# Kernel tuning notes

Hardware: AMD Instinct MI355X
Metric: run time of the kernel (lower is better)

Reference implementation:

```python
import jax, jax.numpy as jnp
import numpy as np

B, L, D, H = 4, 1024, 1024, 16
HS = D // H
BLOCK = 1024
EPS = 1e-5


def setup_inputs() -> dict:
    key = jax.random.key(0)
    ks = jax.random.split(key, 12)
    s = 0.02
    return {
        "x": jax.random.normal(ks[0], (B, L, D), jnp.float32),
        "ln1_w": jnp.ones((D,), jnp.float32),
        "ln1_b": jnp.zeros((D,), jnp.float32),
        "Wqkv": jax.random.normal(ks[1], (D, 3 * D), jnp.float32) * s,
        "bqkv": jnp.zeros((3 * D,), jnp.float32),
        "Wproj": jax.random.normal(ks[2], (D, D), jnp.float32) * s,
        "bproj": jnp.zeros((D,), jnp.float32),
        "Er": jax.random.normal(ks[3], (BLOCK, HS), jnp.float32) * s,
        "ln2_w": jnp.ones((D,), jnp.float32),
        "ln2_b": jnp.zeros((D,), jnp.float32),
        "Wfc": jax.random.normal(ks[4], (D, 4 * D), jnp.float32) * s,
        "bfc": jnp.zeros((4 * D,), jnp.float32),
        "Wfc2": jax.random.normal(ks[5], (4 * D, D), jnp.float32) * s,
        "bfc2": jnp.zeros((D,), jnp.float32),
    }


def _layernorm(x, w, b):
    mu = jnp.mean(x, axis=-1, keepdims=True)
    var = jnp.mean(jnp.square(x - mu), axis=-1, keepdims=True)
    return (x - mu) * jax.lax.rsqrt(var + EPS) * w + b


def _skew(QEr):
    # Music-Transformer skew: pad one zero column on the left of last dim,
    # reshape (B,H,L,L+1) -> (B,H,L+1,L), drop first row.
    b, h, l, _ = QEr.shape
    padded = jnp.pad(QEr, ((0, 0), (0, 0), (0, 0), (1, 0)))
    return padded.reshape(b, h, l + 1, l)[:, :, 1:, :]


def _block(x, ln1_w, ln1_b, Wqkv, bqkv, Wproj, bproj, Er,
           ln2_w, ln2_b, Wfc, bfc, Wfc2, bfc2):
    b, l, d = x.shape
    # --- attention on ln_1(x) ---
    h = _layernorm(x, ln1_w, ln1_b)
    qkv = h @ Wqkv + bqkv                      # (B, L, 3D)
    q, k, v = jnp.split(qkv, 3, axis=-1)
    q = q.reshape(b, l, H, HS).transpose(0, 2, 1, 3)  # (B,H,L,hs)
    k = k.reshape(b, l, H, HS).transpose(0, 2, 1, 3)
    v = v.reshape(b, l, H, HS).transpose(0, 2, 1, 3)

    start = BLOCK - l
    Er_t = Er[start:, :].T                     # (hs, L)
    QEr = jnp.einsum('bhld,dm->bhlm', q, Er_t)  # (B,H,L,L)
    Srel = _skew(QEr)

    QKt = jnp.einsum('bhld,bhmd->bhlm', q, k)  # (B,H,L,L)
    scale = 1.0 / jnp.sqrt(jnp.asarray(HS, x.dtype))
    att = (QKt + Srel) * scale
    causal = jnp.tril(jnp.ones((l, l), bool))
    att = jnp.where(causal, att, jnp.asarray(-jnp.inf, att.dtype))
    att = jax.nn.softmax(att, axis=-1)
    y = jnp.einsum('bhlm,bhmd->bhld', att, v)  # (B,H,L,hs)
    y = y.transpose(0, 2, 1, 3).reshape(b, l, d)
    a = y @ Wproj + bproj

    x = x + a
    # --- MLP on ln_2(x) ---
    h2 = _layernorm(x, ln2_w, ln2_b)
    m = jax.nn.gelu(h2 @ Wfc + bfc, approximate=False) @ Wfc2 + bfc2
    return x + m


def reference(x, ln1_w, ln1_b, Wqkv, bqkv, Wproj, bproj, Er,
              ln2_w, ln2_b, Wfc, bfc, Wfc2, bfc2):
    return _block(x, ln1_w, ln1_b, Wqkv, bqkv, Wproj, bproj, Er,
                  ln2_w, ln2_b, Wfc, bfc, Wfc2, bfc2)
```

## Files before the change

### kernel.cpp

```cpp
#include <hip/hip_runtime.h>
#include <hip/hip_bf16.h>
#include <math.h>

typedef __attribute__((ext_vector_type(8))) __bf16 bf16x8;
typedef __attribute__((ext_vector_type(4))) float f32x4;

#define LL 1024
#define DD 1024
#define HH 16

#define GLOAD16(g, l)                                              \
  __builtin_amdgcn_global_load_lds(                                \
      (const __attribute__((address_space(1))) void*)(g),          \
      (__attribute__((address_space(3))) void*)(l), 16, 0, 0)

#define FENCE asm volatile("" ::: "memory")
#define BARRIER do { FENCE; __builtin_amdgcn_s_barrier(); FENCE; } while (0)
#define SCHEDB __builtin_amdgcn_sched_barrier(0)

__global__ __launch_bounds__(256) void transpose_cvt(const float* __restrict__ W,
                                                     __hip_bfloat16* __restrict__ Wt,
                                                     int R, int C) {
  __shared__ float tile[32][33];
  int tx = threadIdx.x;
  int r0 = blockIdx.y * 32, c0 = blockIdx.x * 32;
  int r = tx >> 3, c4 = (tx & 7) * 4;
  float4 v = *(const float4*)&W[(size_t)(r0 + r) * C + c0 + c4];
  tile[r][c4 + 0] = v.x; tile[r][c4 + 1] = v.y;
  tile[r][c4 + 2] = v.z; tile[r][c4 + 3] = v.w;
  __syncthreads();
  int c = tx >> 3, r4 = (tx & 7) * 4;
  __hip_bfloat16 o[4];
#pragma unroll
  for (int j = 0; j < 4; ++j) o[j] = __float2bfloat16(tile[r4 + j][c]);
  *(uint2*)&Wt[(size_t)(c0 + c) * R + r0 + r4] = *(const uint2*)o;
}

__global__ __launch_bounds__(256) void cvt_er(const float* __restrict__ Er,
                                              __hip_bfloat16* __restrict__ Erb) {
  int i = blockIdx.x * 256 + threadIdx.x;
  float4 v = *(const float4*)&Er[(size_t)i * 4];
  __hip_bfloat16 o[4];
  o[0] = __float2bfloat16(v.x); o[1] = __float2bfloat16(v.y);
  o[2] = __float2bfloat16(v.z); o[3] = __float2bfloat16(v.w);
  *(uint2*)&Erb[(size_t)i * 4] = *(const uint2*)o;
}

__global__ __launch_bounds__(256) void ln_kernel(const float* __restrict__ X,
                                                 const float* __restrict__ w,
                                                 const float* __restrict__ b,
                                                 __hip_bfloat16* __restrict__ out) {
  int row = blockIdx.x;
  int tid = threadIdx.x;
  const float* xr = X + (size_t)row * DD;
  float4 v = *(const float4*)&xr[tid * 4];
  float s = v.x + v.y + v.z + v.w;
  float s2 = v.x * v.x + v.y * v.y + v.z * v.z + v.w * v.w;
#pragma unroll
  for (int m = 1; m < 64; m <<= 1) {
    s += __shfl_xor(s, m);
    s2 += __shfl_xor(s2, m);
  }
  __shared__ float ps[4], ps2[4];
  int wv_ = tid >> 6, lane = tid & 63;
  if (lane == 0) { ps[wv_] = s; ps2[wv_] = s2; }
  __syncthreads();
  float ts = ps[0] + ps[1] + ps[2] + ps[3];
  float ts2 = ps2[0] + ps2[1] + ps2[2] + ps2[3];
  float mu = ts * (1.0f / DD);
  float var = ts2 * (1.0f / DD) - mu * mu;
  float rs = rsqrtf(var + 1e-5f);
  float4 wv = *(const float4*)&w[tid * 4];
  float4 bv = *(const float4*)&b[tid * 4];
  __hip_bfloat16 o[4];
  o[0] = __float2bfloat16((v.x - mu) * rs * wv.x + bv.x);
  o[1] = __float2bfloat16((v.y - mu) * rs * wv.y + bv.y);
  o[2] = __float2bfloat16((v.z - mu) * rs * wv.z + bv.z);
  o[3] = __float2bfloat16((v.w - mu) * rs * wv.w + bv.w);
  *(uint2*)&out[(size_t)row * DD + tid * 4] = *(const uint2*)o;
}

template <int EPI>
__global__ __launch_bounds__(512, 4) void gemm256x128(const __hip_bfloat16* __restrict__ A,
                                                      const __hip_bfloat16* __restrict__ Bt,
                                                      const float* __restrict__ bias,
                                                      const float* __restrict__ resid,
                                                      void* __restrict__ Cout,
                                                      int M, int N, int K) {
  __shared__ __hip_bfloat16 Ab[3][256][32];
  __shared__ __hip_bfloat16 Bb[3][128][32];
  const int tid = threadIdx.x, lane = tid & 63, w = tid >> 6;
  const int wm = w >> 1, wn = w & 1;

  int nbx = gridDim.x, nwg = nbx * gridDim.y;
  int orig = blockIdx.y * nbx + blockIdx.x;
  int cpx = nwg >> 3;
  int wgid = (orig & 7) * cpx + (orig >> 3);
  int bm0 = (wgid / nbx) * 256, bn0 = (wgid % nbx) * 128;

  const int fr = lane & 15, kq = lane >> 4;
  const int sg = ((lane & 3) ^ ((lane >> 3) & 3)) * 8;
  const int srw = lane >> 2;

  auto stageA = [&](int c, int g, int k0) {
    int u = w * 2 + g;
    const __hip_bfloat16* src = A + (size_t)(bm0 + u * 16 + srw) * K + k0 + sg;
    GLOAD16(src, (char*)Ab + c * 16384 + u * 1024);
  };
  auto stageB = [&](int c, int k0) {
    const __hip_bfloat16* src = Bt + (size_t)(bn0 + w * 16 + srw) * K + k0 + sg;
    GLOAD16(src, (char*)Bb + c * 8192 + w * 1024);
  };
  const int swz = ((kq ^ ((fr >> 1) & 3)) << 4);
  auto ldA = [&](int c, int r) -> bf16x8 {
    return *(const bf16x8*)((const char*)Ab + c * 16384 + r * 64 + swz);
  };
  auto ldB = [&](int c, int r) -> bf16x8 {
    return *(const bf16x8*)((const char*)Bb + c * 8192 + r * 64 + swz);
  };

  f32x4 acc[4][4] = {};
  bf16x8 a[4], b[4];

  const int nt = K >> 5;
#pragma unroll
  for (int tt = 0; tt < 2; ++tt) {
    stageA(tt, 0, tt * 32); stageA(tt, 1, tt * 32); stageB(tt, tt * 32);
  }
  asm volatile("s_waitcnt vmcnt(3)" ::: "memory");
  BARRIER;

  int cur = 0, nxt = 2;
  for (int t = 0; t < nt; ++t) {
#pragma unroll
    for (int mf = 0; mf < 4; ++mf) a[mf] = ldA(cur, wm * 64 + mf * 16 + fr);
#pragma unroll
    for (int nf = 0; nf < 4; ++nf) b[nf] = ldB(cur, wn * 64 + nf * 16 + fr);
    if (t + 2 < nt) {
      stageA(nxt, 0, (t + 2) * 32); stageA(nxt, 1, (t + 2) * 32); stageB(nxt, (t + 2) * 32);
    }
    __builtin_amdgcn_s_setprio(1);
#pragma unroll
    for (int mf = 0; mf < 4; ++mf)
#pragma unroll
      for (int nf = 0; nf < 4; ++nf)
        acc[mf][nf] = __builtin_amdgcn_mfma_f32_16x16x32_bf16(a[mf], b[nf], acc[mf][nf], 0, 0, 0);
    __builtin_amdgcn_s_setprio(0);
    if (t <= nt - 3)      { asm volatile("s_waitcnt vmcnt(3)" ::: "memory"); }
    else if (t == nt - 2) { asm volatile("s_waitcnt vmcnt(0)" ::: "memory"); }
    BARRIER;
    cur = (cur == 2) ? 0 : cur + 1;
    nxt = (nxt == 2) ? 0 : nxt + 1;
  }

#pragma unroll
  for (int nf = 0; nf < 4; ++nf) {
    int col = bn0 + wn * 64 + nf * 16 + fr;
    float bsv = bias[col];
#pragma unroll
    for (int mf = 0; mf < 4; ++mf) {
      int rowb = bm0 + wm * 64 + mf * 16 + kq * 4;
#pragma unroll
      for (int j = 0; j < 4; ++j) {
        int row = rowb + j;
        float v = acc[mf][nf][j] + bsv;
        if (EPI == 1) v = 0.5f * v * (1.0f + erff(v * 0.7071067811865476f));
        if (EPI == 2) {
          ((float*)Cout)[(size_t)row * N + col] = v + resid[(size_t)row * N + col];
        } else {
          ((__hip_bfloat16*)Cout)[(size_t)row * N + col] = __float2bfloat16(v);
        }
      }
    }
  }
}

template <int EPI>
__global__ __launch_bounds__(512, 4) void gemm128x64w8(const __hip_bfloat16* __restrict__ A,
                                                       const __hip_bfloat16* __restrict__ Bt,
                                                       const float* __restrict__ bias,
                                                       const float* __restrict__ resid,
                                                       void* __restrict__ Cout,
                                                       int M, int N, int K) {
  __shared__ __hip_bfloat16 Ab[3][128][64];
  __shared__ __hip_bfloat16 Bb[3][64][64];
  const int tid = threadIdx.x, lane = tid & 63, w = tid >> 6;
  const int wm = w >> 1, wn = w & 1;

  int nbx = gridDim.x, nwg = nbx * gridDim.y;
  int orig = blockIdx.y * nbx + blockIdx.x;
  int cpx = nwg >> 3;
  int wgid = (orig & 7) * cpx + (orig >> 3);
  int bm0 = (wgid / nbx) * 128, bn0 = (wgid % nbx) * 64;

  const int fr = lane & 15, kq = lane >> 4;
  const int srw = lane >> 3;
  const int sg = ((lane & 7) ^ (lane >> 3)) * 8;

  auto stageA = [&](int c, int j, int k0) {
    int u = 2 * w + j;
    const __hip_bfloat16* src = A + (size_t)(bm0 + u * 8 + srw) * K + k0 + sg;
    GLOAD16(src, (char*)Ab + c * 16384 + u * 1024);
  };
  auto stageB = [&](int c, int k0) {
    const __hip_bfloat16* src = Bt + (size_t)(bn0 + w * 8 + srw) * K + k0 + sg;
    GLOAD16(src, (char*)Bb + c * 8192 + w * 1024);
  };
  auto ldA = [&](int c, int r, int ks) -> bf16x8 {
    int byte = r * 128 + ((ks * 64 + kq * 16) ^ ((r & 7) << 4));
    return *(const bf16x8*)((const char*)Ab + c * 16384 + byte);
  };
  auto ldB = [&](int c, int r, int ks) -> bf16x8 {
    int byte = r * 128 + ((ks * 64 + kq * 16) ^ ((r & 7) << 4));
    return *(const bf16x8*)((const char*)Bb + c * 8192 + byte);
  };

  f32x4 acc[2][2] = {};
  bf16x8 a[2][2], b[2][2];

  const int nt = K >> 6;
#pragma unroll
  for (int tt = 0; tt < 2; ++tt) {
    stageA(tt, 0, tt * 64); stageA(tt, 1, tt * 64); stageB(tt, tt * 64);
  }
  asm volatile("s_waitcnt vmcnt(3)" ::: "memory");
  BARRIER;

  int cur = 0, nxt = 2;
  for (int t = 0; t < nt; ++t) {
#pragma unroll
    for (int mf = 0; mf < 2; ++mf)
#pragma unroll
      for (int ks = 0; ks < 2; ++ks)
        a[mf][ks] = ldA(cur, wm * 32 + mf * 16 + fr, ks);
#pragma unroll
    for (int nf = 0; nf < 2; ++nf)
#pragma unroll
      for (int ks = 0; ks < 2; ++ks)
        b[nf][ks] = ldB(cur, wn * 32 + nf * 16 + fr, ks);
    if (t + 2 < nt) {
      stageA(nxt, 0, (t + 2) * 64); stageA(nxt, 1, (t + 2) * 64); stageB(nxt, (t + 2) * 64);
    }
    __builtin_amdgcn_s_setprio(1);
#pragma unroll
    for (int mf = 0; mf < 2; ++mf)
#pragma unroll
      for (int nf = 0; nf < 2; ++nf)
#pragma unroll
        for (int ks = 0; ks < 2; ++ks)
          acc[mf][nf] = __builtin_amdgcn_mfma_f32_16x16x32_bf16(
              a[mf][ks], b[nf][ks], acc[mf][nf], 0, 0, 0);
    __builtin_amdgcn_s_setprio(0);
    if (t <= nt - 3)      { asm volatile("s_waitcnt vmcnt(3)" ::: "memory"); }
    else if (t == nt - 2) { asm volatile("s_waitcnt vmcnt(0)" ::: "memory"); }
    BARRIER;
    cur = (cur == 2) ? 0 : cur + 1;
    nxt = (nxt == 2) ? 0 : nxt + 1;
  }

#pragma unroll
  for (int nf = 0; nf < 2; ++nf) {
    int col = bn0 + wn * 32 + nf * 16 + fr;
    float bsv = bias[col];
#pragma unroll
    for (int mf = 0; mf < 2; ++mf) {
      int rowb = bm0 + wm * 32 + mf * 16 + kq * 4;
#pragma unroll
      for (int j = 0; j < 4; ++j) {
        int row = rowb + j;
        float v = acc[mf][nf][j] + bsv;
        if (EPI == 1) v = 0.5f * v * (1.0f + erff(v * 0.7071067811865476f));
        if (EPI == 2) {
          ((float*)Cout)[(size_t)row * N + col] = v + resid[(size_t)row * N + col];
        } else {
          ((__hip_bfloat16*)Cout)[(size_t)row * N + col] = __float2bfloat16(v);
        }
      }
    }
  }
}

__global__ __launch_bounds__(256) void attn_mfma(const __hip_bfloat16* __restrict__ qkv,
                                                 const __hip_bfloat16* __restrict__ Erb,
                                                 __hip_bfloat16* __restrict__ Y) {
  __shared__ __hip_bfloat16 k_s[64][72];
  __shared__ __hip_bfloat16 er_s[64][72];
  __shared__ __hip_bfloat16 p_s[4][16][72];
  __shared__ __hip_bfloat16 g_s[4][16][132];
  __shared__ __hip_bfloat16 vt_s[64 * 64];

  int bid = blockIdx.x;
  int qi = 15 - (bid >> 6);
  int head = bid & 63;
  int h = head & 15, b = head >> 4;
  int l0 = qi * 64;
  int tid = threadIdx.x, lane = tid & 63, w = tid >> 6;
  const int fr = lane & 15, kq = lane >> 4;

  const __hip_bfloat16* base = qkv + (size_t)b * (LL * 3072) + h * 64;

  bf16x8 qf[2];
  {
    const __hip_bfloat16* q0 = base + (size_t)(l0 + 16 * w + fr) * 3072 + kq * 8;
    qf[0] = *(const bf16x8*)q0;
    qf[1] = *(const bf16x8*)(q0 + 32);
  }

  const int ksr = tid >> 2, ksd = (tid & 3) * 16;
  const __hip_bfloat16* ksrc = base + 1024 + (size_t)ksr * 3072 + ksd;
  const int vc = (tid >> 3) * 2, vd0 = (tid & 7) * 8;
  const __hip_bfloat16* vsrc = base + 2048 + (size_t)vc * 3072 + vd0;
  const int err = tid >> 2, erc = (tid & 3) * 16;

  uint4 kst0, kst1, vst0, vst1;
  uint4 ers0, ers1;
  uint4 ec10, ec11;

  {
    kst0 = *(const uint4*)ksrc; kst1 = *(const uint4*)(ksrc + 8);
    vst0 = *(const uint4*)vsrc; vst1 = *(const uint4*)(vsrc + 3072);
    int m0 = min(max(960 - l0 + err, 0), 1023);
    const __hip_bfloat16* ep0 = Erb + (size_t)m0 * 64 + erc;
    ers0 = *(const uint4*)ep0; ers1 = *(const uint4*)(ep0 + 8);
    if (qi > 0) {
      int m1 = min(max(960 - l0 + 64 + err, 0), 1023);
      const __hip_bfloat16* ep1 = Erb + (size_t)m1 * 64 + erc;
      ec10 = *(const uint4*)ep1; ec11 = *(const uint4*)(ep1 + 8);
    }
  }

  f32x4 oacc[4] = {};
  float m_run[4], s_run[4];
#pragma unroll
  for (int j = 0; j < 4; ++j) { m_run[j] = -1e30f; s_run[j] = 0.f; }

  auto gchunk = [&](int hf) {
#pragma unroll
    for (int g = 0; g < 4; ++g) {
      int cc = 16 * g + fr, kc = kq * 8;
      bf16x8 e0 = *(const bf16x8*)&er_s[cc][kc];
      bf16x8 e1 = *(const bf16x8*)&er_s[cc][kc + 32];
      f32x4 gacc = {};
      gacc = __builtin_amdgcn_mfma_f32_16x16x32_bf16(qf[0], e0, gacc, 0, 0, 0);
      gacc = __builtin_amdgcn_mfma_f32_16x16x32_bf16(qf[1], e1, gacc, 0, 0, 0);
#pragma unroll
      for (int j = 0; j < 4; ++j)
        g_s[w][kq * 4 + j][hf * 64 + 16 * g + fr] = __float2bfloat16(gacc[j]);
    }
  };

  for (int t = 0; t <= qi; ++t) {
    __syncthreads();
    *(uint4*)&k_s[ksr][ksd] = kst0;
    *(uint4*)&k_s[ksr][ksd + 8] = kst1;
    {
      const uint16_t* h0 = (const uint16_t*)&vst0;
      const uint16_t* h1 = (const uint16_t*)&vst1;
#pragma unroll
      for (int j = 0; j < 8; ++j) {
        int d = vd0 + j;
        uint32_t pk = (uint32_t)h0[j] | ((uint32_t)h1[j] << 16);
        uint32_t byte = ((uint32_t)d << 7) + 2u * (uint32_t)vc;
        byte ^= (uint32_t)(((d & 7) ^ (d >> 3)) << 4);
        *(uint32_t*)((char*)vt_s + byte) = pk;
      }
    }
    if (t == 0 || t < qi) {
      *(uint4*)&er_s[err][erc]     = ers0;
      *(uint4*)&er_s[err][erc + 8] = ers1;
    }
    __syncthreads();
    if (t < qi) {
      int c0n = (t + 1) * 64;
      const __hip_bfloat16* kp = ksrc + (size_t)c0n * 3072;
      kst0 = *(const uint4*)kp; kst1 = *(const uint4*)(kp + 8);
      const __hip_bfloat16* vp = vsrc + (size_t)c0n * 3072;
      vst0 = *(const uint4*)vp; vst1 = *(const uint4*)(vp + 3072);
      if (t + 1 < qi) {
        int m = min(960 - l0 + (t + 2) * 64 + err, 1023);
        const __hip_bfloat16* ep = Erb + (size_t)m * 64 + erc;
        ers0 = *(const uint4*)ep; ers1 = *(const uint4*)(ep + 8);
      }
    }
    SCHEDB;

    f32x4 sacc[4] = {};
#pragma unroll
    for (int f = 0; f < 4; ++f) {
      int cc = 16 * f + fr, kc = kq * 8;
      bf16x8 k0 = *(const bf16x8*)&k_s[cc][kc];
      bf16x8 k1 = *(const bf16x8*)&k_s[cc][kc + 32];
      sacc[f] = __builtin_amdgcn_mfma_f32_16x16x32_bf16(qf[0], k0, sacc[f], 0, 0, 0);
      sacc[f] = __builtin_amdgcn_mfma_f32_16x16x32_bf16(qf[1], k1, sacc[f], 0, 0, 0);
    }
    if (t == 0) {
      gchunk(0);
      if (qi > 0) {
        __syncthreads();
        *(uint4*)&er_s[err][erc]     = ec10;
        *(uint4*)&er_s[err][erc + 8] = ec11;
        __syncthreads();
        gchunk(1);
      }
    } else if (t < qi) {
      gchunk((t + 1) & 1);
    }

    float sv[4][4];
#pragma unroll
    for (int f = 0; f < 4; ++f) {
#pragma unroll
      for (int j = 0; j < 4; ++j) {
        int r = kq * 4 + j;
        int c = 16 * f + fr;
        int jj = c - (16 * w + r) + 63;
        float g = __bfloat162float(g_s[w][r][(t * 64 + jj) & 127]);
        float val = (sacc[f][j] + g) * 0.125f;
        if (t == qi && c > 16 * w + r) val = -1e30f;
        sv[f][j] = val;
      }
    }
    float alpha[4];
#pragma unroll
    for (int j = 0; j < 4; ++j) {
      float tm = fmaxf(fmaxf(sv[0][j], sv[1][j]), fmaxf(sv[2][j], sv[3][j]));
      tm = fmaxf(tm, __shfl_xor(tm, 1));
      tm = fmaxf(tm, __shfl_xor(tm, 2));
      tm = fmaxf(tm, __shfl_xor(tm, 4));
      tm = fmaxf(tm, __shfl_xor(tm, 8));
      float nm = fmaxf(m_run[j], tm);
      alpha[j] = __expf(m_run[j] - nm);
      m_run[j] = nm;
    }
#pragma unroll
    for (int f = 0; f < 4; ++f)
#pragma unroll
      for (int j = 0; j < 4; ++j)
        sv[f][j] = __expf(sv[f][j] - m_run[j]);
#pragma unroll
    for (int j = 0; j < 4; ++j) {
      float ps = sv[0][j] + sv[1][j] + sv[2][j] + sv[3][j];
      ps += __shfl_xor(ps, 1); ps += __shfl_xor(ps, 2);
      ps += __shfl_xor(ps, 4); ps += __shfl_xor(ps, 8);
      s_run[j] = s_run[j] * alpha[j] + ps;
    }
#pragma unroll
    for (int f = 0; f < 4; ++f)
#pragma unroll
      for (int j = 0; j < 4; ++j)
        oacc[f][j] *= alpha[j];
#pragma unroll
    for (int f = 0; f < 4; ++f)
#pragma unroll
      for (int j = 0; j < 4; ++j)
        p_s[w][kq * 4 + j][16 * f + fr] = __float2bfloat16(sv[f][j]);
#pragma unroll
    for (int kk = 0; kk < 2; ++kk) {
      bf16x8 pf = *(const bf16x8*)&p_s[w][fr][kq * 8 + 32 * kk];
#pragma unroll
      for (int f = 0; f < 4; ++f) {
        int d = 16 * f + fr;
        int cc = kq * 8 + 32 * kk;
        uint32_t byte = ((uint32_t)d << 7) + 2u * (uint32_t)cc;
        byte ^= (uint32_t)(((d & 7) ^ (d >> 3)) << 4);
        bf16x8 vf = *(const bf16x8*)((char*)vt_s + byte);
        oacc[f] = __builtin_amdgcn_mfma_f32_16x16x32_bf16(pf, vf, oacc[f], 0, 0, 0);
      }
    }
  }

#pragma unroll
  for (int f = 0; f < 4; ++f)
#pragma unroll
    for (int j = 0; j < 4; ++j) {
      int r = 16 * w + kq * 4 + j;
      int d = 16 * f + fr;
      float o = oacc[f][j] / s_run[j];
      Y[(size_t)(b * LL + l0 + r) * DD + h * 64 + d] = __float2bfloat16(o);
    }
}

extern "C" void kernel_launch(void* const* d_in, const int* in_sizes, int n_in,
                              void* d_out, int out_size, void* d_ws, size_t ws_size,
                              hipStream_t stream) {
  (void)in_sizes; (void)n_in; (void)out_size; (void)ws_size;
  const float* x     = (const float*)d_in[0];
  const float* ln1w  = (const float*)d_in[1];
  const float* ln1b  = (const float*)d_in[2];
  const float* Wqkv  = (const float*)d_in[3];
  const float* bqkv  = (const float*)d_in[4];
  const float* Wproj = (const float*)d_in[5];
  const float* bproj = (const float*)d_in[6];
  const float* Er    = (const float*)d_in[7];
  const float* ln2w  = (const float*)d_in[8];
  const float* ln2b  = (const float*)d_in[9];
  const float* Wfc   = (const float*)d_in[10];
  const float* bfc   = (const float*)d_in[11];
  const float* Wfc2  = (const float*)d_in[12];
  const float* bfc2  = (const float*)d_in[13];
  float* out = (float*)d_out;

  char* ws = (char*)d_ws;
  const size_t MB = 1ull << 20;
  __hip_bfloat16* h1    = (__hip_bfloat16*)(ws + 0);
  __hip_bfloat16* qkvb  = (__hip_bfloat16*)(ws + 8 * MB);
  __hip_bfloat16* mbuf  = (__hip_bfloat16*)(ws + 0);
  __hip_bfloat16* yb    = (__hip_bfloat16*)(ws + 32 * MB);
  __hip_bfloat16* h2    = (__hip_bfloat16*)(ws + 32 * MB);
  float*          x2    = (float*)(ws + 40 * MB);
  __hip_bfloat16* Wqkvt = (__hip_bfloat16*)(ws + 56 * MB);
  __hip_bfloat16* Erb   = (__hip_bfloat16*)(ws + 62 * MB);
  __hip_bfloat16* Wprojt= (__hip_bfloat16*)(ws + 63 * MB);
  __hip_bfloat16* Wfct  = (__hip_bfloat16*)(ws + 66 * MB);
  __hip_bfloat16* Wfc2t = (__hip_bfloat16*)(ws + 75 * MB);

  dim3 blk(256);

  transpose_cvt<<<dim3(3072 / 32, 1024 / 32), blk, 0, stream>>>(Wqkv, Wqkvt, 1024, 3072);
  transpose_cvt<<<dim3(1024 / 32, 1024 / 32), blk, 0, stream>>>(Wproj, Wprojt, 1024, 1024);
  transpose_cvt<<<dim3(4096 / 32, 1024 / 32), blk, 0, stream>>>(Wfc, Wfct, 1024, 4096);
  transpose_cvt<<<dim3(1024 / 32, 4096 / 32), blk, 0, stream>>>(Wfc2, Wfc2t, 4096, 1024);
  cvt_er<<<dim3(64), blk, 0, stream>>>(Er, Erb);

  ln_kernel<<<4096, blk, 0, stream>>>(x, ln1w, ln1b, h1);

  gemm256x128<0><<<dim3(3072 / 128, 4096 / 256), dim3(512), 0, stream>>>(
      h1, Wqkvt, bqkv, nullptr, qkvb, 4096, 3072, 1024);

  attn_mfma<<<dim3(1024), blk, 0, stream>>>(qkvb, Erb, yb);

  gemm128x64w8<2><<<dim3(1024 / 64, 4096 / 128), dim3(512), 0, stream>>>(
      yb, Wprojt, bproj, x, x2, 4096, 1024, 1024);

  ln_kernel<<<4096, blk, 0, stream>>>(x2, ln2w, ln2b, h2);

  gemm256x128<1><<<dim3(4096 / 128, 4096 / 256), dim3(512), 0, stream>>>(
      h2, Wfct, bfc, nullptr, mbuf, 4096, 4096, 1024);

  gemm128x64w8<2><<<dim3(1024 / 64, 4096 / 128), dim3(512), 0, stream>>>(
      mbuf, Wfc2t, bfc2, x2, out, 4096, 1024, 4096);
}
```

Baseline: 226.0 us.

## Replace direct global-to-LDS loads with register-staged prefetch in GEMM kernels

Both bf16 GEMM kernels stop using global_load_lds. They now load each next tile into registers two steps ahead and write it into a triple-buffered LDS slot one step ahead. The per-iteration vmcnt waits become an lgkmcnt(0) wait plus a barrier. The aim is to avoid stalls and limits tied to the direct LDS load path. The cost is extra VGPRs and LDS write instructions, and each register write must wait for its global load to finish.

```diff
diff --git a/kernel.cpp b/kernel.cpp
--- a/kernel.cpp
+++ b/kernel.cpp
@@ -9,14 +9,10 @@
 #define DD 1024
 #define HH 16
 
-#define GLOAD16(g, l)                                              \
-  __builtin_amdgcn_global_load_lds(                                \
-      (const __attribute__((address_space(1))) void*)(g),          \
-      (__attribute__((address_space(3))) void*)(l), 16, 0, 0)
-
 #define FENCE asm volatile("" ::: "memory")
-#define BARRIER do { FENCE; __builtin_amdgcn_s_barrier(); FENCE; } while (0)
 #define SCHEDB __builtin_amdgcn_sched_barrier(0)
+#define LGKM0_BAR do { FENCE; asm volatile("s_waitcnt lgkmcnt(0)" ::: "memory"); \
+                       __builtin_amdgcn_s_barrier(); FENCE; } while (0)
 
 __global__ __launch_bounds__(256) void transpose_cvt(const float* __restrict__ W,
                                                      __hip_bfloat16* __restrict__ Wt,
@@ -102,14 +98,19 @@
   const int sg = ((lane & 3) ^ ((lane >> 3) & 3)) * 8;
   const int srw = lane >> 2;
 
-  auto stageA = [&](int c, int g, int k0) {
-    int u = w * 2 + g;
-    const __hip_bfloat16* src = A + (size_t)(bm0 + u * 16 + srw) * K + k0 + sg;
-    GLOAD16(src, (char*)Ab + c * 16384 + u * 1024);
-  };
-  auto stageB = [&](int c, int k0) {
-    const __hip_bfloat16* src = Bt + (size_t)(bn0 + w * 16 + srw) * K + k0 + sg;
-    GLOAD16(src, (char*)Bb + c * 8192 + w * 1024);
+  auto ldgA = [&](int j, int k0) -> uint4 {
+    int u = w * 2 + j;
+    return *(const uint4*)(A + (size_t)(bm0 + u * 16 + srw) * K + k0 + sg);
+  };
+  auto ldgB = [&](int k0) -> uint4 {
+    return *(const uint4*)(Bt + (size_t)(bn0 + w * 16 + srw) * K + k0 + sg);
+  };
+  auto wrA = [&](int c, int j, uint4 v) {
+    int u = w * 2 + j;
+    *(uint4*)((char*)Ab + c * 16384 + u * 1024 + lane * 16) = v;
+  };
+  auto wrB = [&](int c, uint4 v) {
+    *(uint4*)((char*)Bb + c * 8192 + w * 1024 + lane * 16) = v;
   };
   const int swz = ((kq ^ ((fr >> 1) & 3)) << 4);
   auto ldA = [&](int c, int r) -> bf16x8 {
@@ -121,24 +122,27 @@
 
   f32x4 acc[4][4] = {};
   bf16x8 a[4], b[4];
+  uint4 sa0, sa1, sb;
 
   const int nt = K >> 5;
-#pragma unroll
-  for (int tt = 0; tt < 2; ++tt) {
-    stageA(tt, 0, tt * 32); stageA(tt, 1, tt * 32); stageB(tt, tt * 32);
-  }
-  asm volatile("s_waitcnt vmcnt(3)" ::: "memory");
-  BARRIER;
-
-  int cur = 0, nxt = 2;
+  sa0 = ldgA(0, 0); sa1 = ldgA(1, 0); sb = ldgB(0);
+  wrA(0, 0, sa0); wrA(0, 1, sa1); wrB(0, sb);
+  sa0 = ldgA(0, 32); sa1 = ldgA(1, 32); sb = ldgB(32);
+  LGKM0_BAR;
+
   for (int t = 0; t < nt; ++t) {
+    int wb = (t + 1) % 3;
+    if (t + 1 < nt) { wrA(wb, 0, sa0); wrA(wb, 1, sa1); wrB(wb, sb); }
+    if (t + 2 < nt) {
+      int kn = (t + 2) * 32;
+      sa0 = ldgA(0, kn); sa1 = ldgA(1, kn); sb = ldgB(kn);
+    }
+    SCHEDB;
+    int cur = t % 3;
 #pragma unroll
     for (int mf = 0; mf < 4; ++mf) a[mf] = ldA(cur, wm * 64 + mf * 16 + fr);
 #pragma unroll
     for (int nf = 0; nf < 4; ++nf) b[nf] = ldB(cur, wn * 64 + nf * 16 + fr);
-    if (t + 2 < nt) {
-      stageA(nxt, 0, (t + 2) * 32); stageA(nxt, 1, (t + 2) * 32); stageB(nxt, (t + 2) * 32);
-    }
     __builtin_amdgcn_s_setprio(1);
 #pragma unroll
     for (int mf = 0; mf < 4; ++mf)
@@ -146,11 +150,7 @@
       for (int nf = 0; nf < 4; ++nf)
         acc[mf][nf] = __builtin_amdgcn_mfma_f32_16x16x32_bf16(a[mf], b[nf], acc[mf][nf], 0, 0, 0);
     __builtin_amdgcn_s_setprio(0);
-    if (t <= nt - 3)      { asm volatile("s_waitcnt vmcnt(3)" ::: "memory"); }
-    else if (t == nt - 2) { asm volatile("s_waitcnt vmcnt(0)" ::: "memory"); }
-    BARRIER;
-    cur = (cur == 2) ? 0 : cur + 1;
-    nxt = (nxt == 2) ? 0 : nxt + 1;
+    LGKM0_BAR;
   }
 
 #pragma unroll
@@ -197,14 +197,19 @@
   const int srw = lane >> 3;
   const int sg = ((lane & 7) ^ (lane >> 3)) * 8;
 
-  auto stageA = [&](int c, int j, int k0) {
+  auto ldgA = [&](int j, int k0) -> uint4 {
     int u = 2 * w + j;
-    const __hip_bfloat16* src = A + (size_t)(bm0 + u * 8 + srw) * K + k0 + sg;
-    GLOAD16(src, (char*)Ab + c * 16384 + u * 1024);
-  };
-  auto stageB = [&](int c, int k0) {
-    const __hip_bfloat16* src = Bt + (size_t)(bn0 + w * 8 + srw) * K + k0 + sg;
-    GLOAD16(src, (char*)Bb + c * 8192 + w * 1024);
+    return *(const uint4*)(A + (size_t)(bm0 + u * 8 + srw) * K + k0 + sg);
+  };
+  auto ldgB = [&](int k0) -> uint4 {
+    return *(const uint4*)(Bt + (size_t)(bn0 + w * 8 + srw) * K + k0 + sg);
+  };
+  auto wrA = [&](int c, int j, uint4 v) {
+    int u = 2 * w + j;
+    *(uint4*)((char*)Ab + c * 16384 + u * 1024 + lane * 16) = v;
+  };
+  auto wrB = [&](int c, uint4 v) {
+    *(uint4*)((char*)Bb + c * 8192 + w * 1024 + lane * 16) = v;
   };
   auto ldA = [&](int c, int r, int ks) -> bf16x8 {
     int byte = r * 128 + ((ks * 64 + kq * 16) ^ ((r & 7) << 4));
@@ -217,17 +222,23 @@
 
   f32x4 acc[2][2] = {};
   bf16x8 a[2][2], b[2][2];
+  uint4 sa0, sa1, sb;
 
   const int nt = K >> 6;
-#pragma unroll
-  for (int tt = 0; tt < 2; ++tt) {
-    stageA(tt, 0, tt * 64); stageA(tt, 1, tt * 64); stageB(tt, tt * 64);
-  }
-  asm volatile("s_waitcnt vmcnt(3)" ::: "memory");
-  BARRIER;
-
-  int cur = 0, nxt = 2;
+  sa0 = ldgA(0, 0); sa1 = ldgA(1, 0); sb = ldgB(0);
+  wrA(0, 0, sa0); wrA(0, 1, sa1); wrB(0, sb);
+  sa0 = ldgA(0, 64); sa1 = ldgA(1, 64); sb = ldgB(64);
+  LGKM0_BAR;
+
   for (int t = 0; t < nt; ++t) {
+    int wb = (t + 1) % 3;
+    if (t + 1 < nt) { wrA(wb, 0, sa0); wrA(wb, 1, sa1); wrB(wb, sb); }
+    if (t + 2 < nt) {
+      int kn = (t + 2) * 64;
+      sa0 = ldgA(0, kn); sa1 = ldgA(1, kn); sb = ldgB(kn);
+    }
+    SCHEDB;
+    int cur = t % 3;
 #pragma unroll
     for (int mf = 0; mf < 2; ++mf)
 #pragma unroll
@@ -238,9 +249,6 @@
 #pragma unroll
       for (int ks = 0; ks < 2; ++ks)
         b[nf][ks] = ldB(cur, wn * 32 + nf * 16 + fr, ks);
-    if (t + 2 < nt) {
-      stageA(nxt, 0, (t + 2) * 64); stageA(nxt, 1, (t + 2) * 64); stageB(nxt, (t + 2) * 64);
-    }
     __builtin_amdgcn_s_setprio(1);
 #pragma unroll
     for (int mf = 0; mf < 2; ++mf)
@@ -251,11 +259,7 @@
           acc[mf][nf] = __builtin_amdgcn_mfma_f32_16x16x32_bf16(
               a[mf][ks], b[nf][ks], acc[mf][nf], 0, 0, 0);
     __builtin_amdgcn_s_setprio(0);
-    if (t <= nt - 3)      { asm volatile("s_waitcnt vmcnt(3)" ::: "memory"); }
-    else if (t == nt - 2) { asm volatile("s_waitcnt vmcnt(0)" ::: "memory"); }
-    BARRIER;
-    cur = (cur == 2) ? 0 : cur + 1;
-    nxt = (nxt == 2) ? 0 : nxt + 1;
+    LGKM0_BAR;
   }
 
 #pragma unroll
```

Result: slower. 237.6 us (+5.1%).
